# Performance work log

Measured on AMD Instinct MI355X. Metric: run time of the kernel, lower is better.

## Reference

```python
import jax, jax.numpy as jnp
import numpy as np

N_SRC = 16384   # src nodes in block (includes dst nodes first, per DGL convention)
N_DST = 8192    # dst nodes
K = 32          # fixed in-degree per dst node -> dense mailbox [N_DST, K]
E = N_DST * K   # 262144 edges; edge i has dst node i // K
T = 16          # padded edge-sequence length
NODE_IN = 64
H = 64          # node_hidden_dim
E_IN = 8        # edge_in_dim
TH = 8          # time_hidden_dim
D_IN = E_IN + TH


def lstm_last(x, lengths, Wih, Whh, bih, bhh):
    """Unidirectional 1-layer LSTM; returns hidden state at step lengths-1 (pack_padded h_n).
    x: (E, T, D); lengths: (E,) in [1, T]. PyTorch gate order: i, f, g, o."""
    n, t_max, _ = x.shape
    h0 = jnp.zeros((n, H), x.dtype)

    def step(carry, xt):
        h, c, hlast, t = carry
        g = xt @ Wih.T + bih + h @ Whh.T + bhh
        i, f, gg, o = jnp.split(g, 4, axis=-1)
        c = jax.nn.sigmoid(f) * c + jax.nn.sigmoid(i) * jnp.tanh(gg)
        h = jax.nn.sigmoid(o) * jnp.tanh(c)
        hlast = jnp.where((t < lengths)[:, None], h, hlast)
        return (h, c, hlast, t + 1), None

    init = (h0, h0, h0, jnp.int32(0))
    (_, _, hlast, _), _ = jax.lax.scan(step, init, jnp.swapaxes(x, 0, 1))
    return hlast  # (E, H)


def sparsemax(z):
    """Sparsemax over last axis (Martins & Astudillo), matching the torch code."""
    z = z - jnp.max(z, axis=-1, keepdims=True)
    zs = -jnp.sort(-z, axis=-1)  # descending
    r = jnp.arange(1, z.shape[-1] + 1, dtype=z.dtype)
    bound = 1.0 + r * zs
    cs = jnp.cumsum(zs, axis=-1)
    is_gt = (bound > cs).astype(z.dtype)
    k = jnp.max(is_gt * r, axis=-1, keepdims=True)
    taus = (jnp.sum(is_gt * zs, axis=-1, keepdims=True) - 1.0) / k
    return jnp.maximum(z - taus, 0.0)


def setup_inputs():
    key = jax.random.key(0)
    ks = jax.random.split(key, 24)
    s = 0.1
    inp = {}
    inp["node_features"] = jax.random.normal(ks[0], (N_SRC, NODE_IN), jnp.float32)
    inp["edge_feats"] = jax.random.normal(ks[1], (E, T, E_IN), jnp.float32)
    inp["e_times"] = jax.random.uniform(ks[2], (E, T), jnp.float32)
    inp["e_len"] = jax.random.randint(ks[3], (E,), 1, T + 1).astype(jnp.int32)
    inp["edge_src"] = jax.random.randint(ks[4], (E,), 0, N_SRC).astype(jnp.int32)
    # Time2Vec (SineActivation) params: v = cat([sin(tau@w + b), tau@w0 + b0])
    inp["t2v_w"] = s * jax.random.normal(ks[5], (1, TH - 1), jnp.float32)
    inp["t2v_b"] = s * jax.random.normal(ks[6], (1, TH - 1), jnp.float32)
    inp["t2v_w0"] = s * jax.random.normal(ks[7], (1, 1), jnp.float32)
    inp["t2v_b0"] = s * jax.random.normal(ks[8], (1, 1), jnp.float32)
    # edge_layer LSTM
    inp["lstm_e_Wih"] = s * jax.random.normal(ks[9], (4 * H, D_IN), jnp.float32)
    inp["lstm_e_Whh"] = s * jax.random.normal(ks[10], (4 * H, H), jnp.float32)
    inp["lstm_e_bih"] = s * jax.random.normal(ks[11], (4 * H,), jnp.float32)
    inp["lstm_e_bhh"] = s * jax.random.normal(ks[12], (4 * H,), jnp.float32)
    # edge_attn_layer LSTM
    inp["lstm_a_Wih"] = s * jax.random.normal(ks[13], (4 * H, D_IN), jnp.float32)
    inp["lstm_a_Whh"] = s * jax.random.normal(ks[14], (4 * H, H), jnp.float32)
    inp["lstm_a_bih"] = s * jax.random.normal(ks[15], (4 * H,), jnp.float32)
    inp["lstm_a_bhh"] = s * jax.random.normal(ks[16], (4 * H,), jnp.float32)
    # attention scorer (no bias), edge_out and node linears
    inp["attn_w"] = s * jax.random.normal(ks[17], (H, 1), jnp.float32)
    inp["edge_out_W"] = s * jax.random.normal(ks[18], (H, NODE_IN + H), jnp.float32)
    inp["edge_out_b"] = s * jax.random.normal(ks[19], (H,), jnp.float32)
    inp["node_W"] = s * jax.random.normal(ks[20], (H, NODE_IN + H), jnp.float32)
    inp["node_b"] = s * jax.random.normal(ks[21], (H,), jnp.float32)
    return inp


def reference(node_features, edge_feats, e_times, t2v_w, t2v_b, t2v_w0, t2v_b0,
              lstm_e_Wih, lstm_e_Whh, lstm_e_bih, lstm_e_bhh,
              lstm_a_Wih, lstm_a_Whh, lstm_a_bih, lstm_a_bhh,
              attn_w, edge_out_W, edge_out_b, node_W, node_b,
              e_len, edge_src):
    h_src = node_features                 # dropout is identity in eval
    h_dst = node_features[:N_DST]
    # Time2Vec: tau (E, T, 1) -> (E, T, TH)
    tau = e_times[..., None]
    tenc = jnp.concatenate([jnp.sin(tau * t2v_w[0] + t2v_b[0]),
                            tau * t2v_w0[0] + t2v_b0[0]], axis=-1)
    e = jnp.concatenate([edge_feats, tenc], axis=-1)  # (E, T, D_IN)
    # per-edge LSTM encodings (last valid step)
    e_out = lstm_last(e, e_len, lstm_e_Wih, lstm_e_Whh, lstm_e_bih, lstm_e_bhh)  # (E, H)
    a_out = lstm_last(e, e_len, lstm_a_Wih, lstm_a_Whh, lstm_a_bih, lstm_a_bhh)  # (E, H)
    a = jax.nn.leaky_relu(a_out @ attn_w, 0.01)  # (E, 1)
    # per-edge message
    m = jax.nn.relu(jnp.concatenate([h_src[edge_src], e_out], axis=-1) @ edge_out_W.T + edge_out_b)  # (E, H)
    # reduce over ragged mailbox (regular degree K -> dense [N_DST, K, H])
    mb = m.reshape(N_DST, K, H)
    alpha = sparsemax(a.reshape(N_DST, K))[..., None]  # (N_DST, K, 1)
    h_neigh = jnp.sum(alpha * mb, axis=1)              # (N_DST, H)
    h = jax.nn.relu(jnp.concatenate([h_dst, h_neigh], axis=-1) @ node_W.T + node_b)
    return h  # (N_DST, H)
```

## Files before the change

### kernel.cpp

```cpp
#include <hip/hip_runtime.h>

typedef __bf16 bf16;
typedef __bf16 bf16x8 __attribute__((ext_vector_type(8)));
typedef float f32x4 __attribute__((ext_vector_type(4)));

#define N_DSTN 8192
#define TT 16
#define HROW 72
#define HBUF (32 * HROW)

#define WS_WHH  0
#define WS_WIH  65536
#define WS_BIAS 81920
#define WS_EW   83968
#define WS_NW   100352
#define WS_EB   116736
#define WS_NB   116992
#define WS_ATTN 117248
#define WS_T2W  117504
#define WS_T2B  117536

__device__ __forceinline__ f32x4 MFMA(bf16x8 a, bf16x8 b, f32x4 c) {
    return __builtin_amdgcn_mfma_f32_16x16x32_bf16(a, b, c, 0, 0, 0);
}
__device__ __forceinline__ float ldf(const void* p, long i, bool isb) {
    return isb ? (float)((const bf16*)p)[i] : ((const float*)p)[i];
}
__device__ __forceinline__ bf16x8 ld8v(const void* p, long i, bool isb) {
    if (isb) {
        return *reinterpret_cast<const bf16x8*>((const bf16*)p + i);
    } else {
        const float* f = (const float*)p + i;
        float4 u = *reinterpret_cast<const float4*>(f);
        float4 v = *reinterpret_cast<const float4*>(f + 4);
        bf16x8 r;
        r[0] = (bf16)u.x; r[1] = (bf16)u.y; r[2] = (bf16)u.z; r[3] = (bf16)u.w;
        r[4] = (bf16)v.x; r[5] = (bf16)v.y; r[6] = (bf16)v.z; r[7] = (bf16)v.w;
        return r;
    }
}

extern "C" __global__ void gtea_prep(const void* __restrict__ e_times,
                                     const void* __restrict__ t2v_w,
                                     const void* __restrict__ t2v_b,
                                     const void* __restrict__ t2v_w0,
                                     const void* __restrict__ t2v_b0,
                                     const void* __restrict__ Wih_e,
                                     const void* __restrict__ Whh_e,
                                     const void* __restrict__ bih_e,
                                     const void* __restrict__ bhh_e,
                                     const void* __restrict__ Wih_a,
                                     const void* __restrict__ Whh_a,
                                     const void* __restrict__ bih_a,
                                     const void* __restrict__ bhh_a,
                                     const void* __restrict__ attn_w,
                                     const void* __restrict__ edge_out_W,
                                     const void* __restrict__ edge_out_b,
                                     const void* __restrict__ node_W,
                                     const void* __restrict__ node_b,
                                     void* __restrict__ ws)
{
    __shared__ int isb_s;
    const int tid = threadIdx.x;
    if (tid < 64) {
        const unsigned short* u = (const unsigned short*)e_times;
        unsigned short a = u[tid * 2], b = u[tid * 2 + 1];
        bool ok = (a <= 0x3F80u) && (b <= 0x3F80u);
        unsigned long long m = __ballot(ok);
        if (tid == 0) isb_s = (m == ~0ULL) ? 1 : 0;
    }
    __syncthreads();
    const bool isb = (isb_s != 0);
    char* wsb = (char*)ws;
    const int gstep = blockDim.x * gridDim.x;
    const int g0 = blockIdx.x * blockDim.x + tid;

    for (int i = g0; i < 2 * 256 * 64; i += gstep) {
        int Lw = i >> 14, rem = i & 16383, n = rem >> 6;
        const void* W = Lw ? Whh_a : Whh_e;
        float gs = ((n >> 6) == 2) ? 2.88539008f : -1.44269504f;
        ((bf16*)(wsb + WS_WHH))[i] = (bf16)(ldf(W, rem, isb) * gs);
    }
    for (int i = g0; i < 2 * 256 * 16; i += gstep) {
        int Lw = i >> 12, rem = i & 4095, n = rem >> 4;
        const void* W = Lw ? Wih_a : Wih_e;
        float gs = ((n >> 6) == 2) ? 2.88539008f : -1.44269504f;
        ((bf16*)(wsb + WS_WIH))[i] = (bf16)(ldf(W, rem, isb) * gs);
    }
    for (int i = g0; i < 2 * 256; i += gstep) {
        int Lw = i >> 8, n = i & 255;
        const void* bi = Lw ? bih_a : bih_e;
        const void* bh = Lw ? bhh_a : bhh_e;
        float gs = ((n >> 6) == 2) ? 2.88539008f : -1.44269504f;
        ((float*)(wsb + WS_BIAS))[i] = (ldf(bi, n, isb) + ldf(bh, n, isb)) * gs;
    }
    for (int i = g0; i < 64 * 128; i += gstep) {
        ((bf16*)(wsb + WS_EW))[i] = (bf16)ldf(edge_out_W, i, isb);
        ((bf16*)(wsb + WS_NW))[i] = (bf16)ldf(node_W, i, isb);
    }
    for (int i = g0; i < 64; i += gstep) {
        ((float*)(wsb + WS_EB))[i]   = ldf(edge_out_b, i, isb);
        ((float*)(wsb + WS_NB))[i]   = ldf(node_b, i, isb);
        ((float*)(wsb + WS_ATTN))[i] = ldf(attn_w, i, isb);
    }
    if (g0 < 7) {
        ((float*)(wsb + WS_T2W))[g0] = ldf(t2v_w, g0, isb);
        ((float*)(wsb + WS_T2B))[g0] = ldf(t2v_b, g0, isb);
    }
    if (g0 == 7) {
        ((float*)(wsb + WS_T2W))[7] = ldf(t2v_w0, 0, isb);
        ((float*)(wsb + WS_T2B))[7] = ldf(t2v_b0, 0, isb);
    }
}

extern "C" __global__ void __launch_bounds__(512, 4)
gtea_fused(const void* __restrict__ node_features,
           const void* __restrict__ edge_feats,
           const void* __restrict__ e_times,
           const int*  __restrict__ e_len,
           const int*  __restrict__ edge_src,
           const void* __restrict__ ws,
           void* __restrict__ outp)
{
    __shared__ __align__(16) bf16 habuf[2][2][HBUF];
    __shared__ __align__(16) bf16 xb[TT * 32 * 16];
    __shared__ __align__(16) bf16 wihb[2 * 256 * 16 + 16];
    __shared__ float t2w[8], t2b[8];
    __shared__ float attn_f[64];
    __shared__ float vbuf[128];
    __shared__ float scores_sh[32], alpha_sh[32];
    __shared__ int   lens_sh[32], idx_sh[32];
    __shared__ int   isb_sh;

    const int tid = threadIdx.x;
    const int w   = tid >> 6;
    const int l   = tid & 63;
    const int l15 = l & 15;
    const int q   = l >> 4;
    const int L   = w >> 2;
    const int w4  = w & 3;
    const int u16 = w4 * 16 + l15;

    const int d  = blockIdx.x;
    const int e0 = d * 32;
    const char* wsb = (const char*)ws;

    if (tid < 64) {
        const unsigned short* u = (const unsigned short*)e_times;
        unsigned short a = u[tid * 2], b = u[tid * 2 + 1];
        bool ok = (a <= 0x3F80u) && (b <= 0x3F80u);
        unsigned long long m = __ballot(ok);
        if (tid == 0) isb_sh = (m == ~0ULL) ? 1 : 0;
    }
    if (tid < 32) {
        int lj = e_len[e0 + tid];
        int rank = 0;
        for (int i = 0; i < 32; i++) {
            int li = __shfl(lj, i);
            rank += (li > lj) || (li == lj && i < tid);
        }
        int mt = rank >> 4, kp = rank & 15;
        int slot = mt * 16 + (kp & 3) * 4 + (kp >> 2);
        idx_sh[slot]  = tid;
        lens_sh[slot] = lj;
    }
    __syncthreads();
    const bool isb = (isb_sh != 0);

    if (tid < 8)  { t2w[tid] = ((const float*)(wsb + WS_T2W))[tid];
                    t2b[tid] = ((const float*)(wsb + WS_T2B))[tid]; }
    if (tid < 64) attn_f[tid] = ((const float*)(wsb + WS_ATTN))[tid];
    if (tid < 64) vbuf[tid] = ldf(node_features, (long)d * 64 + tid, isb);
    {
        unsigned int* hz = reinterpret_cast<unsigned int*>(&habuf[0][0][0]);
        for (int i = tid; i < HBUF / 2; i += 512) { hz[i] = 0u; hz[i + HBUF] = 0u; }
    }
    {
        #pragma unroll
        for (int i = 0; i < 2; i++)
            reinterpret_cast<bf16x8*>(wihb)[tid + i * 512] =
                reinterpret_cast<const bf16x8*>(wsb + WS_WIH)[tid + i * 512];
        if (tid < 16) wihb[2 * 256 * 16 + tid] = (bf16)0.0f;
    }
    __syncthreads();

    int gm0[4], gm1[4];
    #pragma unroll
    for (int r = 0; r < 4; r++) {
        gm0[r] = __builtin_amdgcn_readfirstlane(lens_sh[r]);
        gm1[r] = __builtin_amdgcn_readfirstlane(lens_sh[16 + r]);
    }
    const int tmax = gm0[0], mtmax1 = gm1[0];

    unsigned lp = 0;
    #pragma unroll
    for (int mt = 0; mt < 2; mt++)
        #pragma unroll
        for (int r = 0; r < 4; r++)
            lp |= (unsigned)(lens_sh[mt * 16 + q * 4 + r] - 1) << ((mt * 4 + r) * 4);

    {
        int s = tid >> 4, t = tid & 15;
        int j = idx_sh[s];
        long base = ((long)(e0 + j) * TT + t) * 8;
        *reinterpret_cast<bf16x8*>(&xb[(t * 32 + s) * 16]) = ld8v(edge_feats, base, isb);
        float tau = ldf(e_times, (long)(e0 + j) * TT + t, isb);
        bf16x8 te;
        #pragma unroll
        for (int i = 0; i < 7; i++) te[i] = (bf16)__sinf(tau * t2w[i] + t2b[i]);
        te[7] = (bf16)(tau * t2w[7] + t2b[7]);
        *reinterpret_cast<bf16x8*>(&xb[(t * 32 + s) * 16 + 8]) = te;
    }

    const bf16*  wWhh  = (const bf16*)(wsb + WS_WHH) + (long)L * 256 * 64;
    const float* wBias = (const float*)(wsb + WS_BIAS) + L * 256;
    bf16x8 Bh[4][2];
    float  bias[4];
    #pragma unroll
    for (int j = 0; j < 4; j++) {
        int n = 64 * j + u16;
        Bh[j][0] = *reinterpret_cast<const bf16x8*>(wWhh + (long)n * 64 + q * 8);
        Bh[j][1] = *reinterpret_cast<const bf16x8*>(wWhh + (long)n * 64 + 32 + q * 8);
        bias[j] = wBias[n];
    }

    const bf16* zrow = &wihb[2 * 256 * 16];
    const bf16* bxp  = (q < 2) ? &wihb[(L * 256 + u16) * 16 + q * 8] : zrow;
    const int   bx_str = (q < 2) ? (64 * 16) : 0;
    const bf16* xpt  = (q < 2) ? &xb[l15 * 16 + q * 8] : zrow;
    const int   xa_t = (q < 2) ? (32 * 16) : 0;
    const int   xa_m = (q < 2) ? (16 * 16) : 0;

    float c[2][4];
    #pragma unroll
    for (int mt = 0; mt < 2; mt++)
        #pragma unroll
        for (int r = 0; r < 4; r++) c[mt][r] = 0.0f;

    __syncthreads();

    bf16* hb_base = &habuf[L][0][0];
    const int rd_off = l15 * HROW + q * 8;
    const int wr_off = (q * 4) * HROW + u16;
    const bf16* rp = hb_base + rd_off;
    bf16*       wp = hb_base + HBUF + wr_off;
    const bf16* rpo = hb_base + HBUF + rd_off;
    bf16*       wpo = hb_base + wr_off;

    for (int t = 0; t < tmax; t++) {
        auto do_mt = [&](int mt) {
            const bf16* hr = rp + mt * (16 * HROW);
            bf16x8 ah0 = *reinterpret_cast<const bf16x8*>(hr);
            bf16x8 ah1 = *reinterpret_cast<const bf16x8*>(hr + 32);
            bf16x8 xa  = *reinterpret_cast<const bf16x8*>(xpt + mt * xa_m);
            f32x4 D[4];
            #pragma unroll
            for (int j = 0; j < 4; j++) {
                f32x4 acc = {bias[j], bias[j], bias[j], bias[j]};
                acc = MFMA(ah0, Bh[j][0], acc);
                acc = MFMA(ah1, Bh[j][1], acc);
                bf16x8 bx = *reinterpret_cast<const bf16x8*>(bxp + j * bx_str);
                acc = MFMA(xa, bx, acc);
                D[j] = acc;
            }
            bf16* hw = wp + mt * (16 * HROW);
            #pragma unroll
            for (int r = 0; r < 4; r++) {
                int gmax = mt ? gm1[r] : gm0[r];
                if (t < gmax) {
                    int lm1 = (int)((lp >> ((mt * 4 + r) * 4)) & 15u);
                    if (t <= lm1) {
                        float gi = D[0][r], gf = D[1][r];
                        float gg = D[2][r], go = D[3][r];
                        float ei = __builtin_amdgcn_exp2f(gi);
                        float ef = __builtin_amdgcn_exp2f(gf);
                        float eg = __builtin_amdgcn_exp2f(gg);
                        float di = 1.0f + ei, dfv = 1.0f + ef, dg = 1.0f + eg;
                        float m1 = di * dg;
                        float R1 = __builtin_amdgcn_rcpf(m1 * dfv);
                        float cn = (m1 * R1) * c[mt][r] + (eg - 1.0f) * (dfv * R1);
                        c[mt][r] = cn;
                        float eo = __builtin_amdgcn_exp2f(go);
                        float ec = __builtin_amdgcn_exp2f(2.88539008f * cn);
                        float R2 = __builtin_amdgcn_rcpf((1.0f + eo) * (1.0f + ec));
                        float hn = (ec - 1.0f) * R2;
                        hw[r * HROW] = (bf16)hn;
                    }
                }
            }
        };
        do_mt(0);
        if (t < mtmax1) do_mt(1);
        const bf16* tr = rp; rp = rpo; rpo = tr;
        bf16* tw = wp; wp = wpo; wpo = tw;
        xpt += xa_t;
        __syncthreads();
    }

    if (tid < 256) {
        int s = tid >> 3, c8 = tid & 7;
        const bf16* ha = &habuf[1][lens_sh[s] & 1][s * HROW];
        float p = 0.0f;
        #pragma unroll
        for (int i = 0; i < 8; i++)
            p += (float)ha[c8 * 8 + i] * attn_f[c8 * 8 + i];
        p += __shfl_xor(p, 1);
        p += __shfl_xor(p, 2);
        p += __shfl_xor(p, 4);
        if (c8 == 0) scores_sh[s] = (p > 0.0f) ? p : 0.01f * p;
    }
    float mval[2][4];
    if (tid < 256) {
        const bf16* wEW = (const bf16*)(wsb + WS_EW);
        bf16x8 Bw[4];
        #pragma unroll
        for (int ks = 0; ks < 4; ks++)
            Bw[ks] = *reinterpret_cast<const bf16x8*>(wEW + (long)u16 * 128 + ks * 32 + q * 8);
        float mb = ((const float*)(wsb + WS_EB))[u16];
        #pragma unroll
        for (int mt = 0; mt < 2; mt++) {
            int s = mt * 16 + l15;
            int src = edge_src[e0 + idx_sh[s]];
            bf16x8 a0 = ld8v(node_features, (long)src * 64 + q * 8, isb);
            bf16x8 a1 = ld8v(node_features, (long)src * 64 + 32 + q * 8, isb);
            const bf16* he = &habuf[0][lens_sh[s] & 1][s * HROW];
            bf16x8 a2 = *reinterpret_cast<const bf16x8*>(he + q * 8);
            bf16x8 a3 = *reinterpret_cast<const bf16x8*>(he + 32 + q * 8);
            f32x4 acc = {mb, mb, mb, mb};
            acc = MFMA(a0, Bw[0], acc);
            acc = MFMA(a1, Bw[1], acc);
            acc = MFMA(a2, Bw[2], acc);
            acc = MFMA(a3, Bw[3], acc);
            #pragma unroll
            for (int r = 0; r < 4; r++) mval[mt][r] = fmaxf(acc[r], 0.0f);
        }
    }
    __syncthreads();

    if (tid < 64) {
        float z = (tid < 32) ? scores_sh[tid] : -3.0e38f;
        float zm = z;
        #pragma unroll
        for (int m = 32; m >= 1; m >>= 1) zm = fmaxf(zm, __shfl_xor(zm, m));
        z -= zm;
        int cnt = 0; float sb = 0.0f;
        for (int i = 0; i < 32; i++) {
            float zi = __shfl(z, i);
            bool before = (zi > z) || (zi == z && i < tid);
            if (before) { cnt++; sb += zi; }
        }
        float r = (float)(cnt + 1);
        float S = sb + z;
        bool isgt = (tid < 32) && (1.0f + r * z > S);
        float kf  = isgt ? r : 0.0f;
        float sgt = isgt ? z : 0.0f;
        #pragma unroll
        for (int m = 32; m >= 1; m >>= 1) kf = fmaxf(kf, __shfl_xor(kf, m));
        #pragma unroll
        for (int m = 32; m >= 1; m >>= 1) sgt += __shfl_xor(sgt, m);
        float tau = (sgt - 1.0f) / fmaxf(kf, 1.0f);
        if (tid < 32) alpha_sh[tid] = fmaxf(z - tau, 0.0f);
    }
    __syncthreads();

    if (tid < 256) {
        float hn = 0.0f;
        #pragma unroll
        for (int mt = 0; mt < 2; mt++)
            #pragma unroll
            for (int r = 0; r < 4; r++)
                hn += alpha_sh[mt * 16 + q * 4 + r] * mval[mt][r];
        hn += __shfl_xor(hn, 16);
        hn += __shfl_xor(hn, 32);
        if (q == 0) vbuf[64 + u16] = hn;
    }
    __syncthreads();

    if (tid < 256) {
        int u = tid >> 2, kq = tid & 3;
        const bf16* wNW = (const bf16*)(wsb + WS_NW);
        bf16x8 wv0 = *reinterpret_cast<const bf16x8*>(wNW + (long)u * 128 + kq * 32);
        bf16x8 wv1 = *reinterpret_cast<const bf16x8*>(wNW + (long)u * 128 + kq * 32 + 8);
        bf16x8 wv2 = *reinterpret_cast<const bf16x8*>(wNW + (long)u * 128 + kq * 32 + 16);
        bf16x8 wv3 = *reinterpret_cast<const bf16x8*>(wNW + (long)u * 128 + kq * 32 + 24);
        float acc = 0.0f;
        #pragma unroll
        for (int i = 0; i < 8; i++) {
            acc += (float)wv0[i] * vbuf[kq * 32 + i];
            acc += (float)wv1[i] * vbuf[kq * 32 + 8 + i];
            acc += (float)wv2[i] * vbuf[kq * 32 + 16 + i];
            acc += (float)wv3[i] * vbuf[kq * 32 + 24 + i];
        }
        acc += __shfl_xor(acc, 1);
        acc += __shfl_xor(acc, 2);
        if (kq == 0) {
            float s = acc + ((const float*)(wsb + WS_NB))[u];
            float v = fmaxf(s, 0.0f);
            long o = (long)d * 64 + u;
            if (isb) ((bf16*)outp)[o] = (bf16)v;
            else     ((float*)outp)[o] = v;
        }
    }
}

extern "C" void kernel_launch(void* const* d_in, const int* in_sizes, int n_in,
                              void* d_out, int out_size, void* d_ws, size_t ws_size,
                              hipStream_t stream) {
    gtea_prep<<<32, 256, 0, stream>>>(
        d_in[2],
        d_in[5], d_in[6], d_in[7], d_in[8],
        d_in[9], d_in[10], d_in[11], d_in[12],
        d_in[13], d_in[14], d_in[15], d_in[16],
        d_in[17], d_in[18], d_in[19],
        d_in[20], d_in[21],
        d_ws);
    gtea_fused<<<N_DSTN, 512, 0, stream>>>(
        d_in[0], d_in[1], d_in[2],
        (const int*)d_in[3], (const int*)d_in[4],
        d_ws, d_out);
}
```

Measured before the change: 715.9 us.

## Split fused kernel into per-LSTM blocks and an epilogue kernel with streamed inputs

Splits the single fused kernel into two: an LSTM kernel that runs each of the two LSTMs in its own 256-thread block (twice as many blocks), and an epilogue kernel that does the message matmul, sparsemax and node update. Edge hidden states and attention scores go through global workspace between the kernels. The per-timestep input slab is now prefetched into a double buffer one step ahead, rather than staging all 16 steps up front. The first step skips the recurrent matmul because h is zero. This cuts LDS per block and is meant to raise occupancy and overlap input loads with compute. In exchange it adds an extra launch, global round-trips for the intermediates, and per-timestep prefetch work done by only 8 lanes per wave.

```diff
diff --git a/kernel.cpp b/kernel.cpp
--- a/kernel.cpp
+++ b/kernel.cpp
@@ -19,6 +19,8 @@
 #define WS_ATTN 117248
 #define WS_T2W  117504
 #define WS_T2B  117536
+#define WS_HE   131072
+#define WS_SC   33685504
 
 __device__ __forceinline__ f32x4 MFMA(bf16x8 a, bf16x8 b, f32x4 c) {
     return __builtin_amdgcn_mfma_f32_16x16x32_bf16(a, b, c, 0, 0, 0);
@@ -113,37 +115,29 @@
     }
 }
 
-extern "C" __global__ void __launch_bounds__(512, 4)
-gtea_fused(const void* __restrict__ node_features,
-           const void* __restrict__ edge_feats,
-           const void* __restrict__ e_times,
-           const int*  __restrict__ e_len,
-           const int*  __restrict__ edge_src,
-           const void* __restrict__ ws,
-           void* __restrict__ outp)
+extern "C" __global__ void __launch_bounds__(256, 5)
+gtea_lstm(const void* __restrict__ edge_feats,
+          const void* __restrict__ e_times,
+          const int*  __restrict__ e_len,
+          void* __restrict__ ws)
 {
-    __shared__ __align__(16) bf16 habuf[2][2][HBUF];
-    __shared__ __align__(16) bf16 xb[TT * 32 * 16];
-    __shared__ __align__(16) bf16 wihb[2 * 256 * 16 + 16];
-    __shared__ float t2w[8], t2b[8];
-    __shared__ float attn_f[64];
-    __shared__ float vbuf[128];
-    __shared__ float scores_sh[32], alpha_sh[32];
-    __shared__ int   lens_sh[32], idx_sh[32];
-    __shared__ int   isb_sh;
+    __shared__ __align__(16) bf16 habuf[2][HBUF];
+    __shared__ __align__(16) bf16 xslab[2][32 * 16];
+    __shared__ __align__(16) bf16 wihb[256 * 16 + 16];
+    __shared__ int lens_sh[32], idx_sh[32];
+    __shared__ int isb_sh;
 
     const int tid = threadIdx.x;
-    const int w   = tid >> 6;
+    const int w4  = tid >> 6;
     const int l   = tid & 63;
     const int l15 = l & 15;
     const int q   = l >> 4;
-    const int L   = w >> 2;
-    const int w4  = w & 3;
     const int u16 = w4 * 16 + l15;
 
-    const int d  = blockIdx.x;
-    const int e0 = d * 32;
-    const char* wsb = (const char*)ws;
+    const int g  = blockIdx.x >> 1;
+    const int L  = blockIdx.x & 1;
+    const int e0 = g * 32;
+    char* wsb = (char*)ws;
 
     if (tid < 64) {
         const unsigned short* u = (const unsigned short*)e_times;
@@ -167,23 +161,13 @@
     __syncthreads();
     const bool isb = (isb_sh != 0);
 
-    if (tid < 8)  { t2w[tid] = ((const float*)(wsb + WS_T2W))[tid];
-                    t2b[tid] = ((const float*)(wsb + WS_T2B))[tid]; }
-    if (tid < 64) attn_f[tid] = ((const float*)(wsb + WS_ATTN))[tid];
-    if (tid < 64) vbuf[tid] = ldf(node_features, (long)d * 64 + tid, isb);
-    {
-        unsigned int* hz = reinterpret_cast<unsigned int*>(&habuf[0][0][0]);
-        for (int i = tid; i < HBUF / 2; i += 512) { hz[i] = 0u; hz[i + HBUF] = 0u; }
-    }
-    {
-        #pragma unroll
-        for (int i = 0; i < 2; i++)
-            reinterpret_cast<bf16x8*>(wihb)[tid + i * 512] =
-                reinterpret_cast<const bf16x8*>(wsb + WS_WIH)[tid + i * 512];
-        if (tid < 16) wihb[2 * 256 * 16 + tid] = (bf16)0.0f;
-    }
-    __syncthreads();
-
+    {
+        const bf16x8* src = reinterpret_cast<const bf16x8*>(wsb + WS_WIH) + L * 512;
+        bf16x8* dst = reinterpret_cast<bf16x8*>(wihb);
+        dst[tid]       = src[tid];
+        dst[tid + 256] = src[tid + 256];
+        if (tid < 16) wihb[256 * 16 + tid] = (bf16)0.0f;
+    }
     int gm0[4], gm1[4];
     #pragma unroll
     for (int r = 0; r < 4; r++) {
@@ -198,19 +182,6 @@
         #pragma unroll
         for (int r = 0; r < 4; r++)
             lp |= (unsigned)(lens_sh[mt * 16 + q * 4 + r] - 1) << ((mt * 4 + r) * 4);
-
-    {
-        int s = tid >> 4, t = tid & 15;
-        int j = idx_sh[s];
-        long base = ((long)(e0 + j) * TT + t) * 8;
-        *reinterpret_cast<bf16x8*>(&xb[(t * 32 + s) * 16]) = ld8v(edge_feats, base, isb);
-        float tau = ldf(e_times, (long)(e0 + j) * TT + t, isb);
-        bf16x8 te;
-        #pragma unroll
-        for (int i = 0; i < 7; i++) te[i] = (bf16)__sinf(tau * t2w[i] + t2b[i]);
-        te[7] = (bf16)(tau * t2w[7] + t2b[7]);
-        *reinterpret_cast<bf16x8*>(&xb[(t * 32 + s) * 16 + 8]) = te;
-    }
 
     const bf16*  wWhh  = (const bf16*)(wsb + WS_WHH) + (long)L * 256 * 64;
     const float* wBias = (const float*)(wsb + WS_BIAS) + L * 256;
@@ -224,12 +195,32 @@
         bias[j] = wBias[n];
     }
 
-    const bf16* zrow = &wihb[2 * 256 * 16];
-    const bf16* bxp  = (q < 2) ? &wihb[(L * 256 + u16) * 16 + q * 8] : zrow;
+    auto prefetch_x = [&](int t, int par) {
+        int s = w4 * 8 + (l & 7);
+        int j = idx_sh[s];
+        long base = (long)(e0 + j) * TT + t;
+        bf16x8 f8 = ld8v(edge_feats, base * 8, isb);
+        float tau = ldf(e_times, base, isb);
+        const float* tw = (const float*)(wsb + WS_T2W);
+        const float* tb = (const float*)(wsb + WS_T2B);
+        bf16x8 te;
+        #pragma unroll
+        for (int i = 0; i < 7; i++) te[i] = (bf16)__sinf(tau * tw[i] + tb[i]);
+        te[7] = (bf16)(tau * tw[7] + tb[7]);
+        *reinterpret_cast<bf16x8*>(&xslab[par][s * 16])     = f8;
+        *reinterpret_cast<bf16x8*>(&xslab[par][s * 16 + 8]) = te;
+    };
+    if (l < 8) prefetch_x(0, 0);
+
+    const bf16* zrow   = &wihb[256 * 16];
+    const bf16* bxp    = (q < 2) ? &wihb[u16 * 16 + q * 8] : zrow;
     const int   bx_str = (q < 2) ? (64 * 16) : 0;
-    const bf16* xpt  = (q < 2) ? &xb[l15 * 16 + q * 8] : zrow;
-    const int   xa_t = (q < 2) ? (32 * 16) : 0;
-    const int   xa_m = (q < 2) ? (16 * 16) : 0;
+    const bf16* xbase  = (q < 2) ? &xslab[0][l15 * 16 + q * 8] : zrow;
+    const int   xa_m   = (q < 2) ? (16 * 16) : 0;
+    const int   xa_p   = (q < 2) ? (32 * 16) : 0;
+
+    const int rd_off = l15 * HROW + q * 8;
+    const int wr_off = (q * 4) * HROW + u16;
 
     float c[2][4];
     #pragma unroll
@@ -239,93 +230,153 @@
 
     __syncthreads();
 
-    bf16* hb_base = &habuf[L][0][0];
-    const int rd_off = l15 * HROW + q * 8;
-    const int wr_off = (q * 4) * HROW + u16;
-    const bf16* rp = hb_base + rd_off;
-    bf16*       wp = hb_base + HBUF + wr_off;
-    const bf16* rpo = hb_base + HBUF + rd_off;
-    bf16*       wpo = hb_base + wr_off;
-
-    for (int t = 0; t < tmax; t++) {
-        auto do_mt = [&](int mt) {
-            const bf16* hr = rp + mt * (16 * HROW);
-            bf16x8 ah0 = *reinterpret_cast<const bf16x8*>(hr);
-            bf16x8 ah1 = *reinterpret_cast<const bf16x8*>(hr + 32);
-            bf16x8 xa  = *reinterpret_cast<const bf16x8*>(xpt + mt * xa_m);
+    auto activ = [&](f32x4 (&D)[4], int mt, int r, bf16* hw) {
+        float gi = D[0][r], gf = D[1][r];
+        float gg = D[2][r], go = D[3][r];
+        float ei = __builtin_amdgcn_exp2f(gi);
+        float ef = __builtin_amdgcn_exp2f(gf);
+        float eg = __builtin_amdgcn_exp2f(gg);
+        float di = 1.0f + ei, dfv = 1.0f + ef, dg = 1.0f + eg;
+        float m1 = di * dg;
+        float R1 = __builtin_amdgcn_rcpf(m1 * dfv);
+        float cn = (m1 * R1) * c[mt][r] + (eg - 1.0f) * (dfv * R1);
+        c[mt][r] = cn;
+        float eo = __builtin_amdgcn_exp2f(go);
+        float ec = __builtin_amdgcn_exp2f(2.88539008f * cn);
+        float R2 = __builtin_amdgcn_rcpf((1.0f + eo) * (1.0f + ec));
+        float hn = (ec - 1.0f) * R2;
+        hw[r * HROW] = (bf16)hn;
+    };
+
+    {
+        bf16* wp = &habuf[1][0] + wr_off;
+        #pragma unroll
+        for (int mt = 0; mt < 2; mt++) {
+            bf16x8 xa = *reinterpret_cast<const bf16x8*>(xbase + mt * xa_m);
             f32x4 D[4];
             #pragma unroll
             for (int j = 0; j < 4; j++) {
                 f32x4 acc = {bias[j], bias[j], bias[j], bias[j]};
-                acc = MFMA(ah0, Bh[j][0], acc);
-                acc = MFMA(ah1, Bh[j][1], acc);
                 bf16x8 bx = *reinterpret_cast<const bf16x8*>(bxp + j * bx_str);
                 acc = MFMA(xa, bx, acc);
                 D[j] = acc;
             }
             bf16* hw = wp + mt * (16 * HROW);
             #pragma unroll
-            for (int r = 0; r < 4; r++) {
-                int gmax = mt ? gm1[r] : gm0[r];
-                if (t < gmax) {
-                    int lm1 = (int)((lp >> ((mt * 4 + r) * 4)) & 15u);
-                    if (t <= lm1) {
-                        float gi = D[0][r], gf = D[1][r];
-                        float gg = D[2][r], go = D[3][r];
-                        float ei = __builtin_amdgcn_exp2f(gi);
-                        float ef = __builtin_amdgcn_exp2f(gf);
-                        float eg = __builtin_amdgcn_exp2f(gg);
-                        float di = 1.0f + ei, dfv = 1.0f + ef, dg = 1.0f + eg;
-                        float m1 = di * dg;
-                        float R1 = __builtin_amdgcn_rcpf(m1 * dfv);
-                        float cn = (m1 * R1) * c[mt][r] + (eg - 1.0f) * (dfv * R1);
-                        c[mt][r] = cn;
-                        float eo = __builtin_amdgcn_exp2f(go);
-                        float ec = __builtin_amdgcn_exp2f(2.88539008f * cn);
-                        float R2 = __builtin_amdgcn_rcpf((1.0f + eo) * (1.0f + ec));
-                        float hn = (ec - 1.0f) * R2;
-                        hw[r * HROW] = (bf16)hn;
-                    }
-                }
+            for (int r = 0; r < 4; r++) activ(D, mt, r, hw);
+        }
+        if (l < 8 && 1 < tmax) prefetch_x(1, 1);
+        __syncthreads();
+    }
+
+    auto do_mt = [&](int mt, int t, const bf16* rp, bf16* wp, const bf16* xpt) {
+        const bf16* hr = rp + mt * (16 * HROW);
+        bf16x8 ah0 = *reinterpret_cast<const bf16x8*>(hr);
+        bf16x8 ah1 = *reinterpret_cast<const bf16x8*>(hr + 32);
+        bf16x8 xa  = *reinterpret_cast<const bf16x8*>(xpt + mt * xa_m);
+        f32x4 D[4];
+        #pragma unroll
+        for (int j = 0; j < 4; j++) {
+            f32x4 acc = {bias[j], bias[j], bias[j], bias[j]};
+            acc = MFMA(ah0, Bh[j][0], acc);
+            acc = MFMA(ah1, Bh[j][1], acc);
+            bf16x8 bx = *reinterpret_cast<const bf16x8*>(bxp + j * bx_str);
+            acc = MFMA(xa, bx, acc);
+            D[j] = acc;
+        }
+        bf16* hw = wp + mt * (16 * HROW);
+        #pragma unroll
+        for (int r = 0; r < 4; r++) {
+            int gmax = mt ? gm1[r] : gm0[r];
+            if (t < gmax) {
+                int lm1 = (int)((lp >> ((mt * 4 + r) * 4)) & 15u);
+                if (t <= lm1) activ(D, mt, r, hw);
             }
-        };
-        do_mt(0);
-        if (t < mtmax1) do_mt(1);
-        const bf16* tr = rp; rp = rpo; rpo = tr;
-        bf16* tw = wp; wp = wpo; wpo = tw;
-        xpt += xa_t;
+        }
+    };
+
+    for (int t = 1; t < tmax; t++) {
+        const bf16* rp = &habuf[t & 1][0] + rd_off;
+        bf16*       wp = &habuf[(t + 1) & 1][0] + wr_off;
+        const bf16* xpt = xbase + (t & 1) * xa_p;
+        do_mt(0, t, rp, wp, xpt);
+        if (t < mtmax1) do_mt(1, t, rp, wp, xpt);
+        if (l < 8 && t + 1 < tmax) prefetch_x(t + 1, (t + 1) & 1);
         __syncthreads();
     }
 
-    if (tid < 256) {
+    {
         int s = tid >> 3, c8 = tid & 7;
-        const bf16* ha = &habuf[1][lens_sh[s] & 1][s * HROW];
-        float p = 0.0f;
-        #pragma unroll
-        for (int i = 0; i < 8; i++)
-            p += (float)ha[c8 * 8 + i] * attn_f[c8 * 8 + i];
-        p += __shfl_xor(p, 1);
-        p += __shfl_xor(p, 2);
-        p += __shfl_xor(p, 4);
-        if (c8 == 0) scores_sh[s] = (p > 0.0f) ? p : 0.01f * p;
-    }
+        const bf16* ha = &habuf[lens_sh[s] & 1][s * HROW + c8 * 8];
+        bf16x8 hv = *reinterpret_cast<const bf16x8*>(ha);
+        if (L == 0) {
+            *reinterpret_cast<bf16x8*>((bf16*)(wsb + WS_HE) +
+                ((long)(e0 + idx_sh[s])) * 64 + c8 * 8) = hv;
+        } else {
+            const float* af = (const float*)(wsb + WS_ATTN);
+            float p = 0.0f;
+            #pragma unroll
+            for (int i = 0; i < 8; i++) p += (float)hv[i] * af[c8 * 8 + i];
+            p += __shfl_xor(p, 1);
+            p += __shfl_xor(p, 2);
+            p += __shfl_xor(p, 4);
+            if (c8 == 0)
+                ((float*)(wsb + WS_SC))[e0 + idx_sh[s]] = (p > 0.0f) ? p : 0.01f * p;
+        }
+    }
+}
+
+extern "C" __global__ void __launch_bounds__(256, 4)
+gtea_epi(const void* __restrict__ node_features,
+         const int*  __restrict__ edge_src,
+         const void* __restrict__ e_times,
+         const void* __restrict__ ws,
+         void* __restrict__ outp)
+{
+    __shared__ float vbuf[128];
+    __shared__ float alpha_sh[32];
+    __shared__ int isb_sh;
+
+    const int tid = threadIdx.x;
+    const int w4  = tid >> 6;
+    const int l   = tid & 63;
+    const int l15 = l & 15;
+    const int q   = l >> 4;
+    const int u16 = w4 * 16 + l15;
+
+    const int d  = blockIdx.x;
+    const int e0 = d * 32;
+    const char* wsb = (const char*)ws;
+
+    if (tid < 64) {
+        const unsigned short* u = (const unsigned short*)e_times;
+        unsigned short a = u[tid * 2], b = u[tid * 2 + 1];
+        bool ok = (a <= 0x3F80u) && (b <= 0x3F80u);
+        unsigned long long m = __ballot(ok);
+        if (tid == 0) isb_sh = (m == ~0ULL) ? 1 : 0;
+    }
+    __syncthreads();
+    const bool isb = (isb_sh != 0);
+
+    if (tid < 64) vbuf[tid] = ldf(node_features, (long)d * 64 + tid, isb);
+
     float mval[2][4];
-    if (tid < 256) {
+    {
         const bf16* wEW = (const bf16*)(wsb + WS_EW);
         bf16x8 Bw[4];
         #pragma unroll
         for (int ks = 0; ks < 4; ks++)
             Bw[ks] = *reinterpret_cast<const bf16x8*>(wEW + (long)u16 * 128 + ks * 32 + q * 8);
         float mb = ((const float*)(wsb + WS_EB))[u16];
+        const bf16* hE = (const bf16*)(wsb + WS_HE);
         #pragma unroll
         for (int mt = 0; mt < 2; mt++) {
-            int s = mt * 16 + l15;
-            int src = edge_src[e0 + idx_sh[s]];
+            int e_loc = mt * 16 + l15;
+            int src = edge_src[e0 + e_loc];
             bf16x8 a0 = ld8v(node_features, (long)src * 64 + q * 8, isb);
             bf16x8 a1 = ld8v(node_features, (long)src * 64 + 32 + q * 8, isb);
-            const bf16* he = &habuf[0][lens_sh[s] & 1][s * HROW];
-            bf16x8 a2 = *reinterpret_cast<const bf16x8*>(he + q * 8);
-            bf16x8 a3 = *reinterpret_cast<const bf16x8*>(he + 32 + q * 8);
+            bf16x8 a2 = *reinterpret_cast<const bf16x8*>(hE + (long)(e0 + e_loc) * 64 + q * 8);
+            bf16x8 a3 = *reinterpret_cast<const bf16x8*>(hE + (long)(e0 + e_loc) * 64 + 32 + q * 8);
             f32x4 acc = {mb, mb, mb, mb};
             acc = MFMA(a0, Bw[0], acc);
             acc = MFMA(a1, Bw[1], acc);
@@ -335,10 +386,9 @@
             for (int r = 0; r < 4; r++) mval[mt][r] = fmaxf(acc[r], 0.0f);
         }
     }
-    __syncthreads();
 
     if (tid < 64) {
-        float z = (tid < 32) ? scores_sh[tid] : -3.0e38f;
+        float z = (tid < 32) ? ((const float*)(wsb + WS_SC))[e0 + tid] : -3.0e38f;
         float zm = z;
         #pragma unroll
         for (int m = 32; m >= 1; m >>= 1) zm = fmaxf(zm, __shfl_xor(zm, m));
@@ -363,7 +413,7 @@
     }
     __syncthreads();
 
-    if (tid < 256) {
+    {
         float hn = 0.0f;
         #pragma unroll
         for (int mt = 0; mt < 2; mt++)
@@ -376,7 +426,7 @@
     }
     __syncthreads();
 
-    if (tid < 256) {
+    {
         int u = tid >> 2, kq = tid & 3;
         const bf16* wNW = (const bf16*)(wsb + WS_NW);
         bf16x8 wv0 = *reinterpret_cast<const bf16x8*>(wNW + (long)u * 128 + kq * 32);
@@ -414,8 +464,8 @@
         d_in[17], d_in[18], d_in[19],
         d_in[20], d_in[21],
         d_ws);
-    gtea_fused<<<N_DSTN, 512, 0, stream>>>(
-        d_in[0], d_in[1], d_in[2],
-        (const int*)d_in[3], (const int*)d_in[4],
-        d_ws, d_out);
-}
+    gtea_lstm<<<2 * N_DSTN, 256, 0, stream>>>(
+        d_in[1], d_in[2], (const int*)d_in[3], d_ws);
+    gtea_epi<<<N_DSTN, 256, 0, stream>>>(
+        d_in[0], (const int*)d_in[4], d_in[2], d_ws, d_out);
+}
```

New measurement: 1.456 ms. 103% more time.
